# Kernel tuning notes

Measured on AMD Instinct MI355X. Metric: run time of the kernel, lower is better.

The kernel has to match this reference:

```python
import jax, jax.numpy as jnp
import numpy as np
import math

EMBED_DIM = 1024
N1 = 8192
N2 = 8192

def setup_inputs() -> dict:
    key = jax.random.key(0)
    ks = jax.random.split(key, 16)
    D = EMBED_DIM
    s = 1.0 / math.sqrt(D)
    inp = {
        "input_tensor1": jax.random.normal(ks[0], (N1, D), jnp.float32),
        "input_tensor2": jax.random.normal(ks[1], (N2, D), jnp.float32),
    }
    names = ["q1", "k1", "v1", "q2", "k2", "v2"]
    for i, n in enumerate(names):
        inp[f"W{n}"] = jax.random.normal(ks[2 + 2 * i], (D, D), jnp.float32) * s
        inp[f"b{n}"] = jax.random.normal(ks[3 + 2 * i], (D,), jnp.float32) * 0.01
    return inp

def reference(input_tensor1, input_tensor2,
              Wq1, bq1, Wk1, bk1, Wv1, bv1,
              Wq2, bq2, Wk2, bk2, Wv2, bv2):
    D = Wq1.shape[0]
    scale = 1.0 / math.sqrt(D)
    # projections (torch Linear: x @ W^T + b; here W stored pre-transposed)
    q1 = input_tensor1 @ Wq1 + bq1   # [N1, D]
    k1 = input_tensor1 @ Wk1 + bk1   # [N1, D]
    v1 = input_tensor1 @ Wv1 + bv1   # [N1, D]
    q2 = input_tensor2 @ Wq2 + bq2   # [N2, D]
    k2 = input_tensor2 @ Wk2 + bk2   # [N2, D]
    v2 = input_tensor2 @ Wv2 + bv2   # [N2, D]
    # direction 1: tensor2 queries attend to tensor1 keys/values
    probs1 = jax.nn.sigmoid((q2 @ k1.T) * scale)   # [N2, N1]
    ctx1 = probs1 @ v1                              # [N2, D]
    # direction 2: tensor1 queries attend to tensor2 keys/values
    probs2 = jax.nn.sigmoid((q1 @ k2.T) * scale)   # [N1, N2]
    ctx2 = probs2 @ v2                              # [N1, D]
    return (ctx2, probs2, ctx1, probs1)
```

## Files before the change

kernel.cpp:

```cpp
#include <hip/hip_runtime.h>
#include <hip/hip_bf16.h>

#define DIM   1024
#define NTOK  8192

using bf16 = __hip_bfloat16;
typedef __attribute__((ext_vector_type(8))) short bf16x8;
typedef __attribute__((ext_vector_type(4))) float f32x4;

__device__ __forceinline__ unsigned short f2b(float x) {
  union { __hip_bfloat16 h; unsigned short u; } cv;
  cv.h = __float2bfloat16(x);
  return cv.u;
}

__global__ __launch_bounds__(256) void cast_f32_bf16(const float* __restrict__ in,
                                                     bf16* __restrict__ out, int n4) {
  int i = blockIdx.x * 256 + threadIdx.x;
  if (i < n4) {
    const float4 v = ((const float4*)in)[i];
    ushort4 p;
    p.x = f2b(v.x); p.y = f2b(v.y); p.z = f2b(v.z); p.w = f2b(v.w);
    ((ushort4*)out)[i] = p;
  }
}

__global__ __launch_bounds__(256) void transpose_cast32(const float* __restrict__ in,
                                                        bf16* __restrict__ out, int R, int C) {
  __shared__ float t[32][33];
  const int tilesC = C / 32;
  const int c0 = (blockIdx.x % tilesC) * 32;
  const int r0 = (blockIdx.x / tilesC) * 32;
  const int tx = threadIdx.x & 31, ty = threadIdx.x >> 5;
  #pragma unroll
  for (int i = 0; i < 4; ++i) {
    int r = ty + i * 8;
    t[r][tx] = in[(size_t)(r0 + r) * C + c0 + tx];
  }
  __syncthreads();
  #pragma unroll
  for (int i = 0; i < 4; ++i) {
    int cr = ty + i * 8;
    out[(size_t)(c0 + cr) * R + r0 + tx] = __float2bfloat16(t[tx][cr]);
  }
}

__global__ __launch_bounds__(256) void transpose_bf16(const short* __restrict__ in,
                                                      short* __restrict__ out,
                                                      const short* __restrict__ in2,
                                                      short* __restrict__ out2,
                                                      int R, int C) {
  __shared__ short t[64][72];
  const int tilesC = C >> 6;
  const int tilesPer = (R >> 6) * tilesC;
  int bid = blockIdx.x;
  const short* src = in; short* dst = out;
  if (bid >= tilesPer) { bid -= tilesPer; src = in2; dst = out2; }
  const int r0 = (bid / tilesC) << 6, c0 = (bid % tilesC) << 6;
  const int tr = threadIdx.x >> 3, tc8 = (threadIdx.x & 7) << 3;
  #pragma unroll
  for (int p = 0; p < 2; ++p) {
    int r = tr + p * 32;
    int sc = tc8 ^ (((r >> 3) & 7) << 3);
    *(bf16x8*)&t[r][sc] = *(const bf16x8*)&src[(size_t)(r0 + r) * C + c0 + tc8];
  }
  __syncthreads();
  #pragma unroll
  for (int p = 0; p < 2; ++p) {
    int oc = tr + p * 32;
    bf16x8 v;
    #pragma unroll
    for (int e = 0; e < 8; ++e) {
      int a = tc8 + e;
      v[e] = t[a][oc ^ (((a >> 3) & 7) << 3)];
    }
    *(bf16x8*)&dst[(size_t)(c0 + oc) * R + r0 + tc8] = v;
  }
}

__global__ __launch_bounds__(256) void pack_bias(const float* b0, const float* b1,
                                                 const float* b2, const float* b3,
                                                 const float* b4, const float* b5,
                                                 float* __restrict__ out) {
  int i = blockIdx.x * 256 + threadIdx.x;
  if (i < 6 * DIM) {
    int s = i >> 10, o = i & 1023;
    const float* p = (s == 0) ? b0 : (s == 1) ? b1 : (s == 2) ? b2 : (s == 3) ? b3 : (s == 4) ? b4 : b5;
    out[i] = p[o];
  }
}

template<int EPI, bool DUAL>
__global__ __launch_bounds__(512, 1) void gemm256(
    const bf16* __restrict__ A,  const bf16* __restrict__ Bt,
    const bf16* __restrict__ A2, const bf16* __restrict__ Bt2,
    int M, int N, int K, int tilesN, int perDir,
    const float* __restrict__ bias, const float* __restrict__ bias2, float scale,
    float* __restrict__ Cf, float* __restrict__ Cf2,
    bf16* __restrict__ Cb, bf16* __restrict__ Cb2,
    bf16* __restrict__ Cq, bf16* __restrict__ Ck, bf16* __restrict__ Cv,
    bf16* __restrict__ Cq2, bf16* __restrict__ Ck2, bf16* __restrict__ Cv2)
{
  __shared__ bf16 lds[2][2 * 16384];
  const int t    = threadIdx.x;
  const int lane = t & 63, wid = t >> 6;
  const int wr = wid >> 2, wc = wid & 3;
  const int lr = lane & 15, kg = lane >> 4;

  const int nwg = gridDim.x;
  int bid = blockIdx.x;
  { const int q = nwg >> 3; bid = (bid & 7) * q + (bid >> 3); }

  const bf16* Au = A; const bf16* BtU = Bt;
  float* CfU = Cf; bf16* CbU = Cb;
  if (DUAL && bid >= perDir) { bid -= perDir; Au = A2; BtU = Bt2; CfU = Cf2; CbU = Cb2; }

  const int bm = (bid / tilesN) << 8;
  const int bn = (bid % tilesN) << 8;

  const float* biasU = bias;
  bf16 *CqU = Cq, *CkU = Ck, *CvU = Cv;
  int bmL = bm;
  if (EPI == 5 && bm >= (M >> 1)) {
    BtU = Bt2; biasU = bias2; CqU = Cq2; CkU = Ck2; CvU = Cv2; bmL = bm - (M >> 1);
  }

  const int srow = t >> 3;
  const int scol = ((t & 7) ^ (srow & 7)) * 8;
  const size_t bA = (size_t)(bm + srow) * K + scol;
  const size_t bB = (size_t)(bn + srow) * K + scol;

#define STAGE(buf, isB, R0, tt_) do {                                                   \
    const bf16* g_ = ((isB) ? BtU + bB : Au + bA) + (size_t)(R0) * K + (size_t)(tt_) * 64; \
    __builtin_amdgcn_global_load_lds(                                                   \
        (const __attribute__((address_space(1))) unsigned int*)g_,                      \
        (__attribute__((address_space(3))) unsigned int*)(&lds[buf][((isB) ? 16384 : 0) + (R0) * 64 + t * 8]), \
        16, 0, 0);                                                                      \
  } while (0)

  const int fcol0 = ((kg)     ^ (lr & 7)) * 8;
  const int fcol1 = ((4 + kg) ^ (lr & 7)) * 8;
  const int arow = (wr * 128 + lr) * 64;
  const int brow = (wc * 64 + lr) * 64;

  f32x4 acc[8][4] = {};
  const int NT = K >> 6;

  STAGE(0, false, 0, 0);   STAGE(0, false, 128, 0);
  STAGE(0, false, 64, 0);  STAGE(0, false, 192, 0);
  STAGE(0, true, 0, 0);    STAGE(0, true, 64, 0);
  STAGE(0, true, 128, 0);  STAGE(0, true, 192, 0);
  if (NT > 1) {
    STAGE(1, false, 0, 1); STAGE(1, false, 128, 1);
    STAGE(1, true, 0, 1);  STAGE(1, true, 64, 1);
    asm volatile("s_waitcnt vmcnt(4)" ::: "memory");
  } else {
    asm volatile("s_waitcnt vmcnt(0)" ::: "memory");
  }
  __builtin_amdgcn_sched_barrier(0);
  __builtin_amdgcn_s_barrier();

  for (int tt = 0; tt < NT; ++tt) {
    const int cur = tt & 1;
    const bf16* bufA = &lds[cur][0];
    const bf16* bufB = &lds[cur][16384];
    bf16x8 b0[4], b1[4];

    {
      bf16x8 a0[4], a1[4];
      #pragma unroll
      for (int n = 0; n < 4; ++n) b0[n] = *(const bf16x8*)(bufB + brow + n * 1024 + fcol0);
      #pragma unroll
      for (int n = 0; n < 4; ++n) b1[n] = *(const bf16x8*)(bufB + brow + n * 1024 + fcol1);
      #pragma unroll
      for (int mi = 0; mi < 4; ++mi) a0[mi] = *(const bf16x8*)(bufA + arow + mi * 1024 + fcol0);
      #pragma unroll
      for (int mi = 0; mi < 4; ++mi) a1[mi] = *(const bf16x8*)(bufA + arow + mi * 1024 + fcol1);
      if (tt + 1 < NT) {
        STAGE(cur ^ 1, true, 128, tt + 1); STAGE(cur ^ 1, true, 192, tt + 1);
        STAGE(cur ^ 1, false, 64, tt + 1); STAGE(cur ^ 1, false, 192, tt + 1);
      }
      __builtin_amdgcn_s_barrier();
      asm volatile("s_waitcnt lgkmcnt(0)" ::: "memory");
      __builtin_amdgcn_sched_barrier(0);
      __builtin_amdgcn_s_setprio(1);
      #pragma unroll
      for (int mi = 0; mi < 4; ++mi)
        #pragma unroll
        for (int n = 0; n < 4; ++n)
          acc[mi][n] = __builtin_amdgcn_mfma_f32_16x16x32_bf16(a0[mi], b0[n], acc[mi][n], 0, 0, 0);
      #pragma unroll
      for (int mi = 0; mi < 4; ++mi)
        #pragma unroll
        for (int n = 0; n < 4; ++n)
          acc[mi][n] = __builtin_amdgcn_mfma_f32_16x16x32_bf16(a1[mi], b1[n], acc[mi][n], 0, 0, 0);
      __builtin_amdgcn_s_setprio(0);
      __builtin_amdgcn_s_barrier();
    }
    {
      bf16x8 a0[4], a1[4];
      #pragma unroll
      for (int mi = 0; mi < 4; ++mi) a0[mi] = *(const bf16x8*)(bufA + arow + 4096 + mi * 1024 + fcol0);
      #pragma unroll
      for (int mi = 0; mi < 4; ++mi) a1[mi] = *(const bf16x8*)(bufA + arow + 4096 + mi * 1024 + fcol1);
      if (tt + 2 < NT) {
        STAGE(cur, false, 0, tt + 2); STAGE(cur, false, 128, tt + 2);
        STAGE(cur, true, 0, tt + 2);  STAGE(cur, true, 64, tt + 2);
      }
      __builtin_amdgcn_s_barrier();
      asm volatile("s_waitcnt lgkmcnt(0)" ::: "memory");
      __builtin_amdgcn_sched_barrier(0);
      __builtin_amdgcn_s_setprio(1);
      #pragma unroll
      for (int mi = 0; mi < 4; ++mi)
        #pragma unroll
        for (int n = 0; n < 4; ++n)
          acc[4 + mi][n] = __builtin_amdgcn_mfma_f32_16x16x32_bf16(a0[mi], b0[n], acc[4 + mi][n], 0, 0, 0);
      #pragma unroll
      for (int mi = 0; mi < 4; ++mi)
        #pragma unroll
        for (int n = 0; n < 4; ++n)
          acc[4 + mi][n] = __builtin_amdgcn_mfma_f32_16x16x32_bf16(a1[mi], b1[n], acc[4 + mi][n], 0, 0, 0);
      __builtin_amdgcn_s_setprio(0);
      if (tt + 2 < NT) { asm volatile("s_waitcnt vmcnt(4)" ::: "memory"); }
      else             { asm volatile("s_waitcnt vmcnt(0)" ::: "memory"); }
      __builtin_amdgcn_sched_barrier(0);
      __builtin_amdgcn_s_barrier();
    }
  }
#undef STAGE

  float* Lf = (float*)&lds[0][0];

  float bN[4];
  if (EPI == 5) {
    #pragma unroll
    for (int n = 0; n < 4; ++n) bN[n] = biasU[bn + wc * 64 + n * 16 + lr];
  }

  #pragma unroll
  for (int h = 0; h < 2; ++h) {
    if (wr == h) {
      #pragma unroll
      for (int m = 0; m < 8; ++m)
        #pragma unroll
        for (int n = 0; n < 4; ++n)
          #pragma unroll
          for (int e = 0; e < 4; ++e) {
            const int lrow = kg * 4 + m * 16 + e;
            const int lcol = wc * 64 + n * 16 + lr;
            float v = acc[m][n][e];
            if (EPI == 2 || EPI == 4) v = 1.0f / (1.0f + __expf(-v * scale));
            if (EPI == 5) v += bN[n];
            Lf[lrow * 256 + (lcol ^ (((lrow >> 2) & 3) << 4))] = v;
          }
    }
    __syncthreads();
    #pragma unroll
    for (int rr = 0; rr < 16; ++rr) {
      const int lrow = wid * 16 + rr;
      const int cb   = lane * 4;
      const int cbs  = cb ^ (((lrow >> 2) & 3) << 4);
      const f32x4 v  = *(const f32x4*)&Lf[lrow * 256 + cbs];
      const int gr   = bm + h * 128 + lrow;
      const int gc   = bn + cb;
      if (EPI == 2 || EPI == 4) {
        __builtin_nontemporal_store(v, (f32x4*)&CfU[(size_t)gr * N + gc]);
        if (EPI == 4) {
          ushort4 p; p.x = f2b(v[0]); p.y = f2b(v[1]); p.z = f2b(v[2]); p.w = f2b(v[3]);
          *(ushort4*)&CbU[(size_t)gr * N + gc] = p;
        }
      } else if (EPI == 3) {
        __builtin_nontemporal_store(v, (f32x4*)&CfU[(size_t)gr * N + gc]);
      } else if (EPI == 5) {
        const int seg = bn >> 10;
        const int cl  = (bn & 1023) + cb;
        const int r   = bmL + h * 128 + lrow;
        bf16* sel = (seg == 0) ? CqU : (seg == 1) ? CkU : CvU;
        ushort4 p; p.x = f2b(v[0]); p.y = f2b(v[1]); p.z = f2b(v[2]); p.w = f2b(v[3]);
        *(ushort4*)&sel[(size_t)r * DIM + cl] = p;
      }
    }
    __syncthreads();
  }
}

template<int EPI, bool A_F32>
__global__ __launch_bounds__(256) void gemm_nt(
    const void* __restrict__ Ap, const bf16* __restrict__ Bt,
    int M, int N, int K,
    float scale, float* __restrict__ Cf)
{
  __shared__ bf16 As[128 * 32];
  __shared__ bf16 Bs[128 * 32];
  const int tid  = threadIdx.x;
  const int lane = tid & 63, wid = tid >> 6;
  const int wrr = wid >> 1, wcc = wid & 1;
  const int tilesN = N >> 7;
  const int nwg = gridDim.x;
  int bid = blockIdx.x;
  if ((nwg & 7) == 0) { const int q = nwg >> 3; bid = (bid & 7) * q + (bid >> 3); }
  const int bm = (bid / tilesN) * 128, bn = (bid % tilesN) * 128;
  f32x4 acc[4][4] = {};
  const bf16*  Ab16 = (const bf16*)Ap;
  const float* Af32 = (const float*)Ap;
  const int srow = tid >> 2, sc8 = (tid & 3) * 8;
  const int frow = tid >> 3, fc4 = (tid & 7) * 4;

  for (int k0 = 0; k0 < K; k0 += 32) {
    if (A_F32) {
      #pragma unroll
      for (int is = 0; is < 4; ++is) {
        int row = is * 32 + frow;
        const float4 v = *(const float4*)(Af32 + (size_t)(bm + row) * K + k0 + fc4);
        ushort4 p; p.x = f2b(v.x); p.y = f2b(v.y); p.z = f2b(v.z); p.w = f2b(v.w);
        *(ushort4*)(&As[row * 32 + fc4]) = p;
      }
    } else {
      #pragma unroll
      for (int is = 0; is < 2; ++is) {
        int row = is * 64 + srow;
        const bf16* g = Ab16 + (size_t)(bm + row) * K + k0 + sc8;
        __builtin_amdgcn_global_load_lds(
            (const __attribute__((address_space(1))) unsigned int*)g,
            (__attribute__((address_space(3))) unsigned int*)(&As[row * 32 + sc8]), 16, 0, 0);
      }
    }
    #pragma unroll
    for (int is = 0; is < 2; ++is) {
      int row = is * 64 + srow;
      const bf16* g = Bt + (size_t)(bn + row) * K + k0 + sc8;
      __builtin_amdgcn_global_load_lds(
          (const __attribute__((address_space(1))) unsigned int*)g,
          (__attribute__((address_space(3))) unsigned int*)(&Bs[row * 32 + sc8]), 16, 0, 0);
    }
    __syncthreads();
    const int lrr = lane & 15, kgg = lane >> 4;
    bf16x8 af[4], bfv[4];
    #pragma unroll
    for (int i = 0; i < 4; ++i)
      af[i] = *(const bf16x8*)(&As[(wrr * 64 + i * 16 + lrr) * 32 + kgg * 8]);
    #pragma unroll
    for (int j = 0; j < 4; ++j)
      bfv[j] = *(const bf16x8*)(&Bs[(wcc * 64 + j * 16 + lrr) * 32 + kgg * 8]);
    #pragma unroll
    for (int i = 0; i < 4; ++i)
      #pragma unroll
      for (int j = 0; j < 4; ++j)
        acc[i][j] = __builtin_amdgcn_mfma_f32_16x16x32_bf16(af[i], bfv[j], acc[i][j], 0, 0, 0);
    __syncthreads();
  }
  const int r0 = bm + wrr * 64 + (lane >> 4) * 4;
  const int c0 = bn + wcc * 64 + (lane & 15);
  if (EPI == 2) {
    #pragma unroll
    for (int i = 0; i < 4; ++i)
      #pragma unroll
      for (int j = 0; j < 4; ++j)
        #pragma unroll
        for (int e = 0; e < 4; ++e) {
          float pr = 1.0f / (1.0f + __expf(-acc[i][j][e] * scale));
          Cf[(size_t)(r0 + i * 16 + e) * N + c0 + j * 16] = pr;
        }
  } else {
    #pragma unroll
    for (int i = 0; i < 4; ++i)
      #pragma unroll
      for (int j = 0; j < 4; ++j)
        #pragma unroll
        for (int e = 0; e < 4; ++e)
          Cf[(size_t)(r0 + i * 16 + e) * N + c0 + j * 16] = acc[i][j][e];
  }
}

extern "C" void kernel_launch(void* const* d_in, const int* in_sizes, int n_in,
                              void* d_out, int out_size, void* d_ws, size_t ws_size,
                              hipStream_t stream) {
  const float* x1 = (const float*)d_in[0];
  const float* x2 = (const float*)d_in[1];
  const float* W[6] = { (const float*)d_in[2],  (const float*)d_in[4],  (const float*)d_in[6],
                        (const float*)d_in[8],  (const float*)d_in[10], (const float*)d_in[12] };
  const float* B[6] = { (const float*)d_in[3],  (const float*)d_in[5],  (const float*)d_in[7],
                        (const float*)d_in[9],  (const float*)d_in[11], (const float*)d_in[13] };

  const size_t MD = (size_t)NTOK * DIM;
  const size_t DD = (size_t)DIM * DIM;
  const size_t NN = (size_t)NTOK * NTOK;

  bf16* ws   = (bf16*)d_ws;
  bf16* x1b  = ws;
  bf16* x2b  = x1b + MD;
  bf16* wt1  = x2b + MD;
  bf16* wt2  = wt1 + 3 * DD;
  float* bstack = (float*)(wt2 + 3 * DD);
  bf16* q1   = wt2 + 3 * DD + 16384;
  bf16* k1   = q1 + MD;
  bf16* q2   = k1 + MD;
  bf16* k2   = q2 + MD;
  bf16* v1r  = k2 + MD;
  bf16* v2r  = v1r + MD;
  bf16* v1T  = v2r + MD;
  bf16* v2T  = v1T + MD;
  bf16* probsb = v2T + MD;

  const size_t topBytes = ((size_t)(10 * MD + 6 * DD + 16384) + 2 * NN) * 2;
  const bool top = (ws_size >= topBytes);

  float* out    = (float*)d_out;
  float* ctx2   = out;
  float* probs2 = ctx2 + MD;
  float* ctx1   = probs2 + NN;
  float* probs1 = ctx1 + MD;

  const float scale = 1.0f / 32.0f;

  {
    int n4 = (int)(MD / 4);
    int blks = (n4 + 255) / 256;
    cast_f32_bf16<<<blks, 256, 0, stream>>>(x1, x1b, n4);
    cast_f32_bf16<<<blks, 256, 0, stream>>>(x2, x2b, n4);
  }
  {
    int blks = (DIM / 32) * (DIM / 32);
    transpose_cast32<<<blks, 256, 0, stream>>>(W[0], wt1 + 0 * DD, DIM, DIM);
    transpose_cast32<<<blks, 256, 0, stream>>>(W[1], wt1 + 1 * DD, DIM, DIM);
    transpose_cast32<<<blks, 256, 0, stream>>>(W[2], wt1 + 2 * DD, DIM, DIM);
    transpose_cast32<<<blks, 256, 0, stream>>>(W[3], wt2 + 0 * DD, DIM, DIM);
    transpose_cast32<<<blks, 256, 0, stream>>>(W[4], wt2 + 1 * DD, DIM, DIM);
    transpose_cast32<<<blks, 256, 0, stream>>>(W[5], wt2 + 2 * DD, DIM, DIM);
  }
  pack_bias<<<24, 256, 0, stream>>>(B[0], B[1], B[2], B[3], B[4], B[5], bstack);

  gemm256<5, false><<<64 * 12, 512, 0, stream>>>(
      x1b, wt1, nullptr, wt2, 2 * NTOK, 3 * DIM, DIM, 12, 768,
      bstack, bstack + 3 * DIM, 0.f,
      nullptr, nullptr, nullptr, nullptr,
      q1, k1, v1r, q2, k2, v2r);

  transpose_bf16<<<2 * (NTOK / 64) * (DIM / 64), 256, 0, stream>>>(
      (const short*)v1r, (short*)v1T, (const short*)v2r, (short*)v2T, NTOK, DIM);

  const int perQK = (NTOK / 256) * (NTOK / 256);
  const int perPV = (NTOK / 256) * (DIM / 256);

  if (top) {
    gemm256<4, true><<<2 * perQK, 512, 0, stream>>>(
        q1, k2, q2, k1, NTOK, NTOK, DIM, 32, perQK,
        nullptr, nullptr, scale,
        probs2, probs1, probsb, probsb + NN,
        nullptr, nullptr, nullptr, nullptr, nullptr, nullptr);
    gemm256<3, true><<<2 * perPV, 512, 0, stream>>>(
        probsb, v2T, probsb + NN, v1T, NTOK, DIM, NTOK, 4, perPV,
        nullptr, nullptr, 0.f,
        ctx2, ctx1, nullptr, nullptr,
        nullptr, nullptr, nullptr, nullptr, nullptr, nullptr);
  } else {
    gemm256<2, false><<<perQK, 512, 0, stream>>>(
        q1, k2, nullptr, nullptr, NTOK, NTOK, DIM, 32, perQK,
        nullptr, nullptr, scale,
        probs2, nullptr, nullptr, nullptr,
        nullptr, nullptr, nullptr, nullptr, nullptr, nullptr);
    gemm_nt<3, true><<<(NTOK / 128) * (DIM / 128), 256, 0, stream>>>(
        probs2, v2T, NTOK, DIM, NTOK, 0.f, ctx2);
    gemm256<2, false><<<perQK, 512, 0, stream>>>(
        q2, k1, nullptr, nullptr, NTOK, NTOK, DIM, 32, perQK,
        nullptr, nullptr, scale,
        probs1, nullptr, nullptr, nullptr,
        nullptr, nullptr, nullptr, nullptr, nullptr, nullptr);
    gemm_nt<3, true><<<(NTOK / 128) * (DIM / 128), 256, 0, stream>>>(
        probs1, v1T, NTOK, DIM, NTOK, 0.f, ctx1);
  }
}
```

Measured before the change: 781.0 us.

## Make QK^T gemm persistent over 8 N-tiles with continuous cross-tile prefetch

The gemm256 kernel becomes a flattened loop over TPB output tiles times K-steps, so the QK^T launch uses 256 workgroups that each handle 8 consecutive 256-wide N tiles sharing the same A rows. Global-to-LDS prefetch runs straight across tile boundaries, so the pipeline does not drain and refill per tile, and the epilogue runs in place at each tile end. The epilogue now goes through a separate 32 KB LDS buffer in eight 32-row chunks instead of reusing the operand buffers. This adds LDS use, more barriers per epilogue, and drops the XCD block remapping for the persistent launch, which may change L2 locality.

```diff
diff --git a/kernel.cpp b/kernel.cpp
--- a/kernel.cpp
+++ b/kernel.cpp
@@ -90,7 +90,7 @@
   }
 }
 
-template<int EPI, bool DUAL>
+template<int EPI, bool DUAL, int TPB, int NTLOG>
 __global__ __launch_bounds__(512, 1) void gemm256(
     const bf16* __restrict__ A,  const bf16* __restrict__ Bt,
     const bf16* __restrict__ A2, const bf16* __restrict__ Bt2,
@@ -101,22 +101,30 @@
     bf16* __restrict__ Cq, bf16* __restrict__ Ck, bf16* __restrict__ Cv,
     bf16* __restrict__ Cq2, bf16* __restrict__ Ck2, bf16* __restrict__ Cv2)
 {
+  const int NT = 1 << NTLOG;
+  const int GT = TPB << NTLOG;
   __shared__ bf16 lds[2][2 * 16384];
+  __shared__ float esc[8192];
+
   const int t    = threadIdx.x;
   const int lane = t & 63, wid = t >> 6;
   const int wr = wid >> 2, wc = wid & 3;
   const int lr = lane & 15, kg = lane >> 4;
 
-  const int nwg = gridDim.x;
   int bid = blockIdx.x;
-  { const int q = nwg >> 3; bid = (bid & 7) * q + (bid >> 3); }
+  if (TPB == 1) {
+    const int nwg = gridDim.x;
+    const int q = nwg >> 3;
+    bid = (bid & 7) * q + (bid >> 3);
+  }
+  int g0 = bid * TPB;
 
   const bf16* Au = A; const bf16* BtU = Bt;
   float* CfU = Cf; bf16* CbU = Cb;
-  if (DUAL && bid >= perDir) { bid -= perDir; Au = A2; BtU = Bt2; CfU = Cf2; CbU = Cb2; }
-
-  const int bm = (bid / tilesN) << 8;
-  const int bn = (bid % tilesN) << 8;
+  if (DUAL && g0 >= perDir) { g0 -= perDir; Au = A2; BtU = Bt2; CfU = Cf2; CbU = Cb2; }
+
+  const int bm  = (g0 / tilesN) << 8;
+  const int bn0 = (g0 % tilesN) << 8;
 
   const float* biasU = bias;
   bf16 *CqU = Cq, *CkU = Ck, *CvU = Cv;
@@ -127,15 +135,18 @@
 
   const int srow = t >> 3;
   const int scol = ((t & 7) ^ (srow & 7)) * 8;
-  const size_t bA = (size_t)(bm + srow) * K + scol;
-  const size_t bB = (size_t)(bn + srow) * K + scol;
-
-#define STAGE(buf, isB, R0, tt_) do {                                                   \
-    const bf16* g_ = ((isB) ? BtU + bB : Au + bA) + (size_t)(R0) * K + (size_t)(tt_) * 64; \
-    __builtin_amdgcn_global_load_lds(                                                   \
-        (const __attribute__((address_space(1))) unsigned int*)g_,                      \
-        (__attribute__((address_space(3))) unsigned int*)(&lds[buf][((isB) ? 16384 : 0) + (R0) * 64 + t * 8]), \
-        16, 0, 0);                                                                      \
+  const size_t rA = (size_t)(bm + srow) * K + scol;
+  const size_t rB = (size_t)(bn0 + srow) * K + scol;
+
+#define STAGE(Gi, isB, R0) do {                                                          \
+    const int jj_ = (Gi) >> NTLOG;                                                       \
+    const int tk_ = (Gi) & (NT - 1);                                                     \
+    const bf16* g_ = ((isB) ? BtU + rB + (size_t)jj_ * ((size_t)K << 8) : Au + rA)       \
+                     + (size_t)(R0) * K + (size_t)tk_ * 64;                              \
+    __builtin_amdgcn_global_load_lds(                                                    \
+        (const __attribute__((address_space(1))) unsigned int*)g_,                       \
+        (__attribute__((address_space(3))) unsigned int*)(&lds[(Gi) & 1][((isB) ? 16384 : 0) + (R0) * 64 + t * 8]), \
+        16, 0, 0);                                                                       \
   } while (0)
 
   const int fcol0 = ((kg)     ^ (lr & 7)) * 8;
@@ -144,15 +155,14 @@
   const int brow = (wc * 64 + lr) * 64;
 
   f32x4 acc[8][4] = {};
-  const int NT = K >> 6;
-
-  STAGE(0, false, 0, 0);   STAGE(0, false, 128, 0);
-  STAGE(0, false, 64, 0);  STAGE(0, false, 192, 0);
-  STAGE(0, true, 0, 0);    STAGE(0, true, 64, 0);
-  STAGE(0, true, 128, 0);  STAGE(0, true, 192, 0);
-  if (NT > 1) {
-    STAGE(1, false, 0, 1); STAGE(1, false, 128, 1);
-    STAGE(1, true, 0, 1);  STAGE(1, true, 64, 1);
+
+  STAGE(0, false, 0);   STAGE(0, false, 128);
+  STAGE(0, false, 64);  STAGE(0, false, 192);
+  STAGE(0, true, 0);    STAGE(0, true, 64);
+  STAGE(0, true, 128);  STAGE(0, true, 192);
+  if (GT > 1) {
+    STAGE(1, false, 0); STAGE(1, false, 128);
+    STAGE(1, true, 0);  STAGE(1, true, 64);
     asm volatile("s_waitcnt vmcnt(4)" ::: "memory");
   } else {
     asm volatile("s_waitcnt vmcnt(0)" ::: "memory");
@@ -160,8 +170,8 @@
   __builtin_amdgcn_sched_barrier(0);
   __builtin_amdgcn_s_barrier();
 
-  for (int tt = 0; tt < NT; ++tt) {
-    const int cur = tt & 1;
+  for (int G = 0; G < GT; ++G) {
+    const int cur = G & 1;
     const bf16* bufA = &lds[cur][0];
     const bf16* bufB = &lds[cur][16384];
     bf16x8 b0[4], b1[4];
@@ -176,9 +186,9 @@
       for (int mi = 0; mi < 4; ++mi) a0[mi] = *(const bf16x8*)(bufA + arow + mi * 1024 + fcol0);
       #pragma unroll
       for (int mi = 0; mi < 4; ++mi) a1[mi] = *(const bf16x8*)(bufA + arow + mi * 1024 + fcol1);
-      if (tt + 1 < NT) {
-        STAGE(cur ^ 1, true, 128, tt + 1); STAGE(cur ^ 1, true, 192, tt + 1);
-        STAGE(cur ^ 1, false, 64, tt + 1); STAGE(cur ^ 1, false, 192, tt + 1);
+      if (G + 1 < GT) {
+        STAGE(G + 1, true, 128); STAGE(G + 1, true, 192);
+        STAGE(G + 1, false, 64); STAGE(G + 1, false, 192);
       }
       __builtin_amdgcn_s_barrier();
       asm volatile("s_waitcnt lgkmcnt(0)" ::: "memory");
@@ -203,9 +213,9 @@
       for (int mi = 0; mi < 4; ++mi) a0[mi] = *(const bf16x8*)(bufA + arow + 4096 + mi * 1024 + fcol0);
       #pragma unroll
       for (int mi = 0; mi < 4; ++mi) a1[mi] = *(const bf16x8*)(bufA + arow + 4096 + mi * 1024 + fcol1);
-      if (tt + 2 < NT) {
-        STAGE(cur, false, 0, tt + 2); STAGE(cur, false, 128, tt + 2);
-        STAGE(cur, true, 0, tt + 2);  STAGE(cur, true, 64, tt + 2);
+      if (G + 2 < GT) {
+        STAGE(G + 2, false, 0); STAGE(G + 2, false, 128);
+        STAGE(G + 2, true, 0);  STAGE(G + 2, true, 64);
       }
       __builtin_amdgcn_s_barrier();
       asm volatile("s_waitcnt lgkmcnt(0)" ::: "memory");
@@ -222,67 +232,82 @@
         for (int n = 0; n < 4; ++n)
           acc[4 + mi][n] = __builtin_amdgcn_mfma_f32_16x16x32_bf16(a1[mi], b1[n], acc[4 + mi][n], 0, 0, 0);
       __builtin_amdgcn_s_setprio(0);
-      if (tt + 2 < NT) { asm volatile("s_waitcnt vmcnt(4)" ::: "memory"); }
-      else             { asm volatile("s_waitcnt vmcnt(0)" ::: "memory"); }
+      if (G + 2 < GT) { asm volatile("s_waitcnt vmcnt(4)" ::: "memory"); }
+      else            { asm volatile("s_waitcnt vmcnt(0)" ::: "memory"); }
       __builtin_amdgcn_sched_barrier(0);
       __builtin_amdgcn_s_barrier();
     }
-  }
-#undef STAGE
-
-  float* Lf = (float*)&lds[0][0];
-
-  float bN[4];
-  if (EPI == 5) {
-    #pragma unroll
-    for (int n = 0; n < 4; ++n) bN[n] = biasU[bn + wc * 64 + n * 16 + lr];
-  }
-
-  #pragma unroll
-  for (int h = 0; h < 2; ++h) {
-    if (wr == h) {
+
+    if ((G & (NT - 1)) == NT - 1) {
+      const int j   = G >> NTLOG;
+      const int bnj = bn0 + (j << 8);
+
+      float bN[4];
+      if (EPI == 5) {
+        #pragma unroll
+        for (int n = 0; n < 4; ++n) bN[n] = biasU[bnj + wc * 64 + n * 16 + lr];
+      }
+
+      #pragma unroll
+      for (int p = 0; p < 8; ++p) {
+        const int h = p >> 2;
+        if (wr == h) {
+          #pragma unroll
+          for (int mm = 0; mm < 2; ++mm)
+            #pragma unroll
+            for (int n = 0; n < 4; ++n)
+              #pragma unroll
+              for (int e = 0; e < 4; ++e) {
+                const int rl  = mm * 16 + kg * 4 + e;
+                const int col = wc * 64 + n * 16 + lr;
+                float v = acc[(p & 3) * 2 + mm][n][e];
+                if (EPI == 2 || EPI == 4) v = 1.0f / (1.0f + __expf(-v * scale));
+                if (EPI == 5) v += bN[n];
+                esc[rl * 256 + (col ^ (((rl >> 2) & 3) << 4))] = v;
+              }
+        }
+        asm volatile("s_waitcnt lgkmcnt(0)" ::: "memory");
+        __builtin_amdgcn_sched_barrier(0);
+        __builtin_amdgcn_s_barrier();
+        #pragma unroll
+        for (int rr = 0; rr < 4; ++rr) {
+          const int rl  = wid * 4 + rr;
+          const int cb  = lane * 4;
+          const int cbs = cb ^ (((rl >> 2) & 3) << 4);
+          const f32x4 v = *(const f32x4*)&esc[rl * 256 + cbs];
+          const int gr  = bm + h * 128 + (p & 3) * 32 + rl;
+          const int gc  = bnj + cb;
+          if (EPI == 2 || EPI == 4) {
+            __builtin_nontemporal_store(v, (f32x4*)&CfU[(size_t)gr * N + gc]);
+            if (EPI == 4) {
+              ushort4 pk; pk.x = f2b(v[0]); pk.y = f2b(v[1]); pk.z = f2b(v[2]); pk.w = f2b(v[3]);
+              *(ushort4*)&CbU[(size_t)gr * N + gc] = pk;
+            }
+          } else if (EPI == 3) {
+            __builtin_nontemporal_store(v, (f32x4*)&CfU[(size_t)gr * N + gc]);
+          } else if (EPI == 5) {
+            const int seg = bnj >> 10;
+            const int cl  = (bnj & 1023) + cb;
+            const int r   = bmL + h * 128 + (p & 3) * 32 + rl;
+            bf16* sel = (seg == 0) ? CqU : (seg == 1) ? CkU : CvU;
+            ushort4 pk; pk.x = f2b(v[0]); pk.y = f2b(v[1]); pk.z = f2b(v[2]); pk.w = f2b(v[3]);
+            *(ushort4*)&sel[(size_t)r * DIM + cl] = pk;
+          }
+        }
+        asm volatile("s_waitcnt lgkmcnt(0)" ::: "memory");
+        __builtin_amdgcn_sched_barrier(0);
+        __builtin_amdgcn_s_barrier();
+      }
+
       #pragma unroll
       for (int m = 0; m < 8; ++m)
         #pragma unroll
         for (int n = 0; n < 4; ++n)
           #pragma unroll
-          for (int e = 0; e < 4; ++e) {
-            const int lrow = kg * 4 + m * 16 + e;
-            const int lcol = wc * 64 + n * 16 + lr;
-            float v = acc[m][n][e];
-            if (EPI == 2 || EPI == 4) v = 1.0f / (1.0f + __expf(-v * scale));
-            if (EPI == 5) v += bN[n];
-            Lf[lrow * 256 + (lcol ^ (((lrow >> 2) & 3) << 4))] = v;
-          }
-    }
-    __syncthreads();
-    #pragma unroll
-    for (int rr = 0; rr < 16; ++rr) {
-      const int lrow = wid * 16 + rr;
-      const int cb   = lane * 4;
-      const int cbs  = cb ^ (((lrow >> 2) & 3) << 4);
-      const f32x4 v  = *(const f32x4*)&Lf[lrow * 256 + cbs];
-      const int gr   = bm + h * 128 + lrow;
-      const int gc   = bn + cb;
-      if (EPI == 2 || EPI == 4) {
-        __builtin_nontemporal_store(v, (f32x4*)&CfU[(size_t)gr * N + gc]);
-        if (EPI == 4) {
-          ushort4 p; p.x = f2b(v[0]); p.y = f2b(v[1]); p.z = f2b(v[2]); p.w = f2b(v[3]);
-          *(ushort4*)&CbU[(size_t)gr * N + gc] = p;
-        }
-      } else if (EPI == 3) {
-        __builtin_nontemporal_store(v, (f32x4*)&CfU[(size_t)gr * N + gc]);
-      } else if (EPI == 5) {
-        const int seg = bn >> 10;
-        const int cl  = (bn & 1023) + cb;
-        const int r   = bmL + h * 128 + lrow;
-        bf16* sel = (seg == 0) ? CqU : (seg == 1) ? CkU : CvU;
-        ushort4 p; p.x = f2b(v[0]); p.y = f2b(v[1]); p.z = f2b(v[2]); p.w = f2b(v[3]);
-        *(ushort4*)&sel[(size_t)r * DIM + cl] = p;
-      }
-    }
-    __syncthreads();
-  }
+          for (int e = 0; e < 4; ++e) acc[m][n][e] = 0.0f;
+    }
+  }
+#undef STAGE
 }
 
 template<int EPI, bool A_F32>
@@ -431,7 +456,7 @@
   }
   pack_bias<<<24, 256, 0, stream>>>(B[0], B[1], B[2], B[3], B[4], B[5], bstack);
 
-  gemm256<5, false><<<64 * 12, 512, 0, stream>>>(
+  gemm256<5, false, 1, 4><<<64 * 12, 512, 0, stream>>>(
       x1b, wt1, nullptr, wt2, 2 * NTOK, 3 * DIM, DIM, 12, 768,
       bstack, bstack + 3 * DIM, 0.f,
       nullptr, nullptr, nullptr, nullptr,
@@ -444,25 +469,25 @@
   const int perPV = (NTOK / 256) * (DIM / 256);
 
   if (top) {
-    gemm256<4, true><<<2 * perQK, 512, 0, stream>>>(
+    gemm256<4, true, 8, 4><<<256, 512, 0, stream>>>(
         q1, k2, q2, k1, NTOK, NTOK, DIM, 32, perQK,
         nullptr, nullptr, scale,
         probs2, probs1, probsb, probsb + NN,
         nullptr, nullptr, nullptr, nullptr, nullptr, nullptr);
-    gemm256<3, true><<<2 * perPV, 512, 0, stream>>>(
+    gemm256<3, true, 1, 7><<<2 * perPV, 512, 0, stream>>>(
         probsb, v2T, probsb + NN, v1T, NTOK, DIM, NTOK, 4, perPV,
         nullptr, nullptr, 0.f,
         ctx2, ctx1, nullptr, nullptr,
         nullptr, nullptr, nullptr, nullptr, nullptr, nullptr);
   } else {
-    gemm256<2, false><<<perQK, 512, 0, stream>>>(
+    gemm256<2, false, 1, 4><<<perQK, 512, 0, stream>>>(
         q1, k2, nullptr, nullptr, NTOK, NTOK, DIM, 32, perQK,
         nullptr, nullptr, scale,
         probs2, nullptr, nullptr, nullptr,
         nullptr, nullptr, nullptr, nullptr, nullptr, nullptr);
     gemm_nt<3, true><<<(NTOK / 128) * (DIM / 128), 256, 0, stream>>>(
         probs2, v2T, NTOK, DIM, NTOK, 0.f, ctx2);
-    gemm256<2, false><<<perQK, 512, 0, stream>>>(
+    gemm256<2, false, 1, 4><<<perQK, 512, 0, stream>>>(
         q2, k1, nullptr, nullptr, NTOK, NTOK, DIM, 32, perQK,
         nullptr, nullptr, scale,
         probs1, nullptr, nullptr, nullptr,
```

Result: slower. 911.0 us (+16.6%).
